# Performance work log

Measured on AMD Instinct MI355X. Metric: run time of the kernel, lower is better.

## Reference

```python
import jax, jax.numpy as jnp
import numpy as np


def setup_inputs() -> dict:
    key = jax.random.key(0)
    k1, k2, k3 = jax.random.split(key, 3)
    bs, chart_len, H = 256, 1024, 256
    num_steps, start_index = 512, 512
    chart = jax.random.normal(k1, (bs, chart_len, 2 * H), dtype=jnp.float32)
    operations = jax.random.randint(k2, (num_steps, bs, 2), 0, start_index, dtype=jnp.int64)
    U = jax.random.normal(k3, (5 * H, 2 * H), dtype=jnp.float32) * 0.05
    b = jnp.zeros((5 * H,), dtype=jnp.float32)
    return {"chart": chart, "operations": operations, "start_index": start_index, "U": U, "b": b}


def reference(chart, operations, start_index, U, b):
    H = U.shape[0] // 5
    bs = chart.shape[0]
    batch_idx = jnp.arange(bs)
    num_steps = operations.shape[0]

    def step_fn(ch, xs):
        step, ops = xs
        left = ch[batch_idx, ops[:, 0]]   # [bs, 2H]
        right = ch[batch_idx, ops[:, 1]]  # [bs, 2H]
        ccL, ccR = left[:, :H], right[:, :H]
        hh = jnp.concatenate([left[:, H:], right[:, H:]], axis=-1)  # [bs, 2H]
        preact = hh @ U.T + b  # [bs, 5H]
        i = jax.nn.sigmoid(preact[:, :H])
        fL = jax.nn.sigmoid(preact[:, H:2 * H])
        fR = jax.nn.sigmoid(preact[:, 2 * H:3 * H])
        o = jax.nn.sigmoid(preact[:, 3 * H:4 * H])
        u = jnp.tanh(preact[:, 4 * H:5 * H])
        c = fL * ccL + fR * ccR + i * u
        h = o * jnp.tanh(c)
        ch = ch.at[:, start_index + step, :].set(jnp.concatenate([c, h], axis=-1))
        return ch, None

    chart, _ = jax.lax.scan(step_fn, chart, (jnp.arange(num_steps), operations))
    return chart
```

## Files before the change

### kernel.cpp

```cpp
#include <hip/hip_runtime.h>
#include <hip/hip_bf16.h>

#define H_     256
#define TWOH_  512
#define CL_    1024
#define BS_    256
#define START_ 512

typedef float  f32x16   __attribute__((ext_vector_type(16)));
typedef short  short8_t __attribute__((ext_vector_type(8)));
typedef short  short4_t __attribute__((ext_vector_type(4)));
typedef __bf16 bf16x8   __attribute__((ext_vector_type(8)));

static __device__ __forceinline__ unsigned short f2bf(float x) {
  __hip_bfloat16 h = __float2bfloat16(x);
  return __builtin_bit_cast(unsigned short, h);
}

static __device__ __forceinline__ void gload16(const void* g, void* l) {
  __builtin_amdgcn_global_load_lds(
      (const __attribute__((address_space(1))) void*)g,
      (__attribute__((address_space(3))) void*)l, 16, 0, 0);
}

#define SCHED0() __builtin_amdgcn_sched_barrier(0)

__global__ void uconv_kernel(const float* __restrict__ U,
                             unsigned short* __restrict__ ub) {
  int tid = blockIdx.x * 256 + threadIdx.x;
  if (tid >= 1280 * 512) return;
  int n = tid >> 9, k = tid & 511;
  int g = n >> 8, j = n & 255;
  int jc = j >> 6, c = (g << 6) + (j & 63);
  ub[((jc * 320 + c) << 9) + k] = f2bf(U[tid]);
}

__global__ void hbcopy_kernel(const float4* __restrict__ chart4,
                              float4* __restrict__ out4,
                              unsigned short* __restrict__ hb) {
  const long long total = 16777216LL;
  long long tid = (long long)blockIdx.x * blockDim.x + threadIdx.x;
  for (long long e = tid; e < total; e += (long long)gridDim.x * blockDim.x) {
    long long i   = e >> 16;
    long long rem = e & 65535;
    long long off = (i << 17) + rem;
    float4 f = chart4[off];
    out4[off] = f;
    int col4 = (int)(rem & 127);
    if (col4 >= 64) {
      long long pos = rem >> 7;
      short4_t v;
      v[0] = (short)f2bf(f.x); v[1] = (short)f2bf(f.y);
      v[2] = (short)f2bf(f.z); v[3] = (short)f2bf(f.w);
      *(short4_t*)(hb + ((i * 512 + pos) * 256 + (long long)(col4 - 64) * 4)) = v;
    }
  }
}

__global__ void copy_kernel(const float4* __restrict__ src,
                            float4* __restrict__ dst) {
  long long tid = (long long)blockIdx.x * blockDim.x + threadIdx.x;
  const long long total = 16777216LL;
  for (long long e = tid; e < total; e += (long long)gridDim.x * blockDim.x) {
    long long i   = e >> 16;
    long long rem = e & 65535;
    long long off = (i << 17) + rem;
    dst[off] = src[off];
  }
}

__global__ __launch_bounds__(512, 2) void chart4_kernel(
    const float* __restrict__ chart,
    const int* __restrict__ ops,
    const unsigned short* __restrict__ ub,
    const unsigned short* __restrict__ hb,
    const float* __restrict__ bias,
    float* __restrict__ out)
{
  __shared__ unsigned short As[2][256 * 64];
  __shared__ unsigned short Bs[2][320 * 64];
  __shared__ int opsl[512];

  const int tid = threadIdx.x, lane = tid & 63, wid = tid >> 6;
  const int l31 = lane & 31, lhi = lane >> 5;
  const int wm = wid >> 1, wn = wid & 1;

  const int bx = blockIdx.x;
  const int g  = (bx & 7) * 256 + (bx >> 3);
  const int s  = g >> 2, jc = g & 3;

  opsl[tid] = ops[s * 512 + tid];
  __syncthreads();

  const int arow   = tid >> 3;
  const int slotA  = tid & 7;
  const int chunkA = slotA ^ (arow & 7);
  int opL256[4], opR256[4];
  const unsigned short* hbA[4];
  #pragma unroll
  for (int p = 0; p < 4; ++p) {
    int row = arow + p * 64;
    opL256[p] = opsl[2 * row] * 256;
    opR256[p] = opsl[2 * row + 1] * 256;
    hbA[p] = hb + ((size_t)row * 512) * 256 + chunkA * 8;
  }
  const unsigned short* ubB[5];
  #pragma unroll
  for (int p = 0; p < 5; ++p) {
    int row = arow + p * 64;
    ubB[p] = ub + (((size_t)(jc * 320 + row)) << 9) + chunkA * 8;
  }

  f32x16 acc0[5], acc1[5];
  #pragma unroll
  for (int gg = 0; gg < 5; ++gg)
    #pragma unroll
    for (int q = 0; q < 16; ++q) { acc0[gg][q] = 0.f; acc1[gg][q] = 0.f; }

#define STAGE(BUF, KT) do {                                                     \
    const int koff_ = ((KT) < 4) ? (KT) * 64 : (KT) * 64 - 256;                 \
    _Pragma("unroll")                                                           \
    for (int p = 0; p < 4; ++p) {                                               \
      const unsigned short* g_ =                                                \
          hbA[p] + (((KT) < 4) ? opL256[p] : opR256[p]) + koff_;                \
      gload16(g_, &As[BUF][(p * 512 + tid) * 8]);                               \
    }                                                                           \
    _Pragma("unroll")                                                           \
    for (int p = 0; p < 5; ++p) {                                               \
      gload16(ubB[p] + (KT) * 64, &Bs[BUF][(p * 512 + tid) * 8]);               \
    }                                                                           \
  } while (0)

  const int sw7  = l31 & 7;
  const int aro0 = (wm * 64 + l31) * 64;
  const int aro1 = aro0 + 32 * 64;
  const int bro  = (wn * 32 + l31) * 64;

#define COMPUTE(BUF) do {                                                       \
    _Pragma("unroll")                                                           \
    for (int ks = 0; ks < 4; ++ks) {                                            \
      const int ce = ((ks * 2 + lhi) ^ sw7) * 8;                                \
      bf16x8 a0 = __builtin_bit_cast(bf16x8,                                    \
          *(const short8_t*)&As[BUF][aro0 + ce]);                               \
      bf16x8 a1 = __builtin_bit_cast(bf16x8,                                    \
          *(const short8_t*)&As[BUF][aro1 + ce]);                               \
      _Pragma("unroll")                                                         \
      for (int gg = 0; gg < 5; ++gg) {                                          \
        bf16x8 b = __builtin_bit_cast(bf16x8,                                   \
            *(const short8_t*)&Bs[BUF][bro + gg * 4096 + ce]);                  \
        acc0[gg] = __builtin_amdgcn_mfma_f32_32x32x16_bf16(a0,b,acc0[gg],0,0,0);\
        acc1[gg] = __builtin_amdgcn_mfma_f32_32x32x16_bf16(a1,b,acc1[gg],0,0,0);\
      }                                                                         \
    }                                                                           \
  } while (0)

#define PHASE(BUF, KT, DOSTAGE) do {                                            \
    asm volatile("s_waitcnt vmcnt(9)" ::: "memory");                            \
    __builtin_amdgcn_s_barrier();                                               \
    SCHED0();                                                                   \
    __builtin_amdgcn_s_setprio(1);                                              \
    COMPUTE(BUF);                                                               \
    __builtin_amdgcn_s_setprio(0);                                              \
    SCHED0();                                                                   \
    __builtin_amdgcn_s_barrier();                                               \
    SCHED0();                                                                   \
    if (DOSTAGE) { STAGE(BUF, (KT) + 2); SCHED0(); }                            \
  } while (0)

  STAGE(0, 0); SCHED0();
  STAGE(1, 1); SCHED0();

  #pragma unroll
  for (int kt = 0; kt < 6; kt += 2) {
    PHASE(0, kt,     true);
    PHASE(1, kt + 1, true);
  }
  PHASE(0, 6, false);
  asm volatile("s_waitcnt vmcnt(0)" ::: "memory");
  __builtin_amdgcn_s_barrier();
  SCHED0();
  COMPUTE(1);

#undef PHASE
#undef COMPUTE
#undef STAGE

  const int jlane = jc * 64 + wn * 32 + l31;
  float bg[5];
  #pragma unroll
  for (int gg = 0; gg < 5; ++gg) bg[gg] = bias[gg * H_ + jlane];

#define EPI(ACC, MF) do {                                                       \
    _Pragma("unroll")                                                           \
    for (int q = 0; q < 16; ++q) {                                              \
      const int i_   = wm * 64 + (MF) * 32 + (q & 3) + 8 * (q >> 2) + 4 * lhi;  \
      const int opL_ = opsl[2 * i_], opR_ = opsl[2 * i_ + 1];                   \
      const float ccL_ = chart[((size_t)i_ * CL_ + opL_) * TWOH_ + jlane];      \
      const float ccR_ = chart[((size_t)i_ * CL_ + opR_) * TWOH_ + jlane];      \
      float pi_  = (ACC)[0][q] + bg[0];                                         \
      float pfL_ = (ACC)[1][q] + bg[1];                                         \
      float pfR_ = (ACC)[2][q] + bg[2];                                         \
      float po_  = (ACC)[3][q] + bg[3];                                         \
      float pu_  = (ACC)[4][q] + bg[4];                                         \
      float gi_  = 1.f / (1.f + __expf(-pi_));                                  \
      float gfL_ = 1.f / (1.f + __expf(-pfL_));                                 \
      float gfR_ = 1.f / (1.f + __expf(-pfR_));                                 \
      float go_  = 1.f / (1.f + __expf(-po_));                                  \
      float eu_  = __expf(2.f * pu_);                                           \
      float gu_  = 1.f - 2.f / (eu_ + 1.f);                                     \
      float c_   = gfL_ * ccL_ + gfR_ * ccR_ + gi_ * gu_;                       \
      float ec_  = __expf(2.f * c_);                                            \
      float th_  = 1.f - 2.f / (ec_ + 1.f);                                     \
      float h_   = go_ * th_;                                                   \
      float* orow_ = out + ((size_t)i_ * CL_ + START_ + s) * TWOH_;             \
      orow_[jlane]      = c_;                                                   \
      orow_[H_ + jlane] = h_;                                                   \
    }                                                                           \
  } while (0)

  EPI(acc0, 0);
  EPI(acc1, 1);
#undef EPI
}

__global__ __launch_bounds__(256, 2) void chart1_kernel(
    const float* __restrict__ chart,
    const int* __restrict__ ops,
    const float* __restrict__ U,
    const float* __restrict__ bias,
    float* __restrict__ out)
{
  __shared__ unsigned short As[64 * 72];
  __shared__ unsigned short Bs[320 * 72];
  __shared__ int opsl[128];

  const int tid = threadIdx.x, lane = tid & 63, wid = tid >> 6;
  const int wm = wid & 1, wn = wid >> 1;
  const int bx = blockIdx.x, jc = blockIdx.y;
  const int s = bx >> 2, ibase = (bx & 3) * 64, j0 = jc * 64;

  if (tid < 128) opsl[tid] = ops[(s * BS_ + ibase) * 2 + tid];
  __syncthreads();

  const int arow = tid >> 2, aqc = tid & 3;
  const int opL_s = opsl[2 * arow], opR_s = opsl[2 * arow + 1];
  const long long abase_i = (long long)(ibase + arow) * CL_;

  f32x16 acc[5];
  #pragma unroll
  for (int g = 0; g < 5; ++g)
    #pragma unroll
    for (int q = 0; q < 16; ++q) acc[g][q] = 0.0f;

  const int a_off  = (wm * 32 + (lane & 31)) * 72 + 8 * (lane >> 5);
  const int b_off0 = (wn * 32 + (lane & 31)) * 72 + 8 * (lane >> 5);

  for (int kt = 0; kt < 8; ++kt) {
    const int k0 = kt * 64;
    {
      const int op   = (k0 < 256) ? opL_s : opR_s;
      const int col0 = ((k0 < 256) ? 256 + k0 : k0) + aqc * 16;
      const float* src = chart + (abase_i + op) * TWOH_ + col0;
      float4 f0 = *(const float4*)(src + 0);
      float4 f1 = *(const float4*)(src + 4);
      float4 f2 = *(const float4*)(src + 8);
      float4 f3 = *(const float4*)(src + 12);
      short8_t v0, v1;
      v0[0] = (short)f2bf(f0.x); v0[1] = (short)f2bf(f0.y);
      v0[2] = (short)f2bf(f0.z); v0[3] = (short)f2bf(f0.w);
      v0[4] = (short)f2bf(f1.x); v0[5] = (short)f2bf(f1.y);
      v0[6] = (short)f2bf(f1.z); v0[7] = (short)f2bf(f1.w);
      v1[0] = (short)f2bf(f2.x); v1[1] = (short)f2bf(f2.y);
      v1[2] = (short)f2bf(f2.z); v1[3] = (short)f2bf(f2.w);
      v1[4] = (short)f2bf(f3.x); v1[5] = (short)f2bf(f3.y);
      v1[6] = (short)f2bf(f3.z); v1[7] = (short)f2bf(f3.w);
      *(short8_t*)&As[arow * 72 + aqc * 16]     = v0;
      *(short8_t*)&As[arow * 72 + aqc * 16 + 8] = v1;
    }
    #pragma unroll
    for (int cc = 0; cc < 20; ++cc) {
      int chunk = cc * 256 + tid;
      int c  = chunk >> 4;
      int ko = (chunk & 15) * 4;
      int n  = ((c >> 6) << 8) + j0 + (c & 63);
      float4 f = *(const float4*)(U + (long long)n * 512 + k0 + ko);
      short4_t v;
      v[0] = (short)f2bf(f.x); v[1] = (short)f2bf(f.y);
      v[2] = (short)f2bf(f.z); v[3] = (short)f2bf(f.w);
      *(short4_t*)&Bs[c * 72 + ko] = v;
    }
    __syncthreads();

    #pragma unroll
    for (int ks = 0; ks < 4; ++ks) {
      bf16x8 a = __builtin_bit_cast(bf16x8, *(const short8_t*)&As[a_off + ks * 16]);
      #pragma unroll
      for (int g = 0; g < 5; ++g) {
        bf16x8 b = __builtin_bit_cast(bf16x8,
            *(const short8_t*)&Bs[b_off0 + g * 64 * 72 + ks * 16]);
        acc[g] = __builtin_amdgcn_mfma_f32_32x32x16_bf16(a, b, acc[g], 0, 0, 0);
      }
    }
    __syncthreads();
  }

  const int jlane = j0 + wn * 32 + (lane & 31);
  float bg[5];
  #pragma unroll
  for (int g = 0; g < 5; ++g) bg[g] = bias[g * H_ + jlane];

  #pragma unroll
  for (int q = 0; q < 16; ++q) {
    int rl  = wm * 32 + (q & 3) + 8 * (q >> 2) + 4 * (lane >> 5);
    int i   = ibase + rl;
    int opL = opsl[2 * rl], opR = opsl[2 * rl + 1];
    float ccL = chart[((long long)i * CL_ + opL) * TWOH_ + jlane];
    float ccR = chart[((long long)i * CL_ + opR) * TWOH_ + jlane];
    float pi  = acc[0][q] + bg[0];
    float pfL = acc[1][q] + bg[1];
    float pfR = acc[2][q] + bg[2];
    float po  = acc[3][q] + bg[3];
    float pu  = acc[4][q] + bg[4];
    float gi  = 1.f / (1.f + __expf(-pi));
    float gfL = 1.f / (1.f + __expf(-pfL));
    float gfR = 1.f / (1.f + __expf(-pfR));
    float go  = 1.f / (1.f + __expf(-po));
    float eu  = __expf(2.f * pu);
    float gu  = 1.f - 2.f / (eu + 1.f);
    float c   = gfL * ccL + gfR * ccR + gi * gu;
    float ec  = __expf(2.f * c);
    float th  = 1.f - 2.f / (ec + 1.f);
    float h   = go * th;
    float* orow = out + ((long long)i * CL_ + START_ + s) * TWOH_;
    orow[jlane]      = c;
    orow[H_ + jlane] = h;
  }
}

extern "C" void kernel_launch(void* const* d_in, const int* in_sizes, int n_in,
                              void* d_out, int out_size, void* d_ws, size_t ws_size,
                              hipStream_t stream) {
  const float* chart = (const float*)d_in[0];
  const int*   ops   = (const int*)d_in[1];
  const float* U     = (const float*)d_in[3];
  const float* bias  = (const float*)d_in[4];
  float* out = (float*)d_out;

  const size_t HB_OFF   = (size_t)2 << 20;
  const size_t HB_BYTES = (size_t)256 * 512 * 256 * 2;

  if (ws_size >= HB_OFF + HB_BYTES) {
    unsigned short* ub = (unsigned short*)d_ws;
    unsigned short* hb = (unsigned short*)((char*)d_ws + HB_OFF);
    uconv_kernel<<<2560, 256, 0, stream>>>(U, ub);
    hbcopy_kernel<<<4096, 256, 0, stream>>>((const float4*)chart, (float4*)out, hb);
    chart4_kernel<<<2048, 512, 0, stream>>>(chart, ops, ub, hb, bias, out);
  } else {
    copy_kernel<<<4096, 256, 0, stream>>>((const float4*)chart, (float4*)out);
    chart1_kernel<<<dim3(2048, 4), 256, 0, stream>>>(chart, ops, U, bias, out);
  }
}
```

Before: 407.6 us.

## Loop over all four output column chunks inside one block per step

```diff
diff --git a/kernel.cpp b/kernel.cpp
--- a/kernel.cpp
+++ b/kernel.cpp
@@ -69,7 +69,7 @@
   }
 }
 
-__global__ __launch_bounds__(512, 2) void chart4_kernel(
+__global__ __launch_bounds__(512, 2) void chart5_kernel(
     const float* __restrict__ chart,
     const int* __restrict__ ops,
     const unsigned short* __restrict__ ub,
@@ -84,10 +84,7 @@
   const int tid = threadIdx.x, lane = tid & 63, wid = tid >> 6;
   const int l31 = lane & 31, lhi = lane >> 5;
   const int wm = wid >> 1, wn = wid & 1;
-
-  const int bx = blockIdx.x;
-  const int g  = (bx & 7) * 256 + (bx >> 3);
-  const int s  = g >> 2, jc = g & 3;
+  const int s = blockIdx.x;
 
   opsl[tid] = ops[s * 512 + tid];
   __syncthreads();
@@ -108,16 +105,12 @@
   #pragma unroll
   for (int p = 0; p < 5; ++p) {
     int row = arow + p * 64;
-    ubB[p] = ub + (((size_t)(jc * 320 + row)) << 9) + chunkA * 8;
+    ubB[p] = ub + ((size_t)row << 9) + chunkA * 8;
   }
 
   f32x16 acc0[5], acc1[5];
-  #pragma unroll
-  for (int gg = 0; gg < 5; ++gg)
-    #pragma unroll
-    for (int q = 0; q < 16; ++q) { acc0[gg][q] = 0.f; acc1[gg][q] = 0.f; }
-
-#define STAGE(BUF, KT) do {                                                     \
+
+#define STAGE(BUF, KT, UBO) do {                                                \
     const int koff_ = ((KT) < 4) ? (KT) * 64 : (KT) * 64 - 256;                 \
     _Pragma("unroll")                                                           \
     for (int p = 0; p < 4; ++p) {                                               \
@@ -127,7 +120,7 @@
     }                                                                           \
     _Pragma("unroll")                                                           \
     for (int p = 0; p < 5; ++p) {                                               \
-      gload16(ubB[p] + (KT) * 64, &Bs[BUF][(p * 512 + tid) * 8]);               \
+      gload16(ubB[p] + (UBO) + (KT) * 64, &Bs[BUF][(p * 512 + tid) * 8]);       \
     }                                                                           \
   } while (0)
 
@@ -154,7 +147,7 @@
     }                                                                           \
   } while (0)
 
-#define PHASE(BUF, KT, DOSTAGE) do {                                            \
+#define PHASE(BUF, KT, UBO, DOSTAGE) do {                                       \
     asm volatile("s_waitcnt vmcnt(9)" ::: "memory");                            \
     __builtin_amdgcn_s_barrier();                                               \
     SCHED0();                                                                   \
@@ -164,31 +157,47 @@
     SCHED0();                                                                   \
     __builtin_amdgcn_s_barrier();                                               \
     SCHED0();                                                                   \
-    if (DOSTAGE) { STAGE(BUF, (KT) + 2); SCHED0(); }                            \
+    if (DOSTAGE) { STAGE(BUF, (KT) + 2, UBO); SCHED0(); }                       \
   } while (0)
 
-  STAGE(0, 0); SCHED0();
-  STAGE(1, 1); SCHED0();
-
-  #pragma unroll
-  for (int kt = 0; kt < 6; kt += 2) {
-    PHASE(0, kt,     true);
-    PHASE(1, kt + 1, true);
-  }
-  PHASE(0, 6, false);
-  asm volatile("s_waitcnt vmcnt(0)" ::: "memory");
-  __builtin_amdgcn_s_barrier();
-  SCHED0();
-  COMPUTE(1);
-
-#undef PHASE
-#undef COMPUTE
-#undef STAGE
-
-  const int jlane = jc * 64 + wn * 32 + l31;
-  float bg[5];
-  #pragma unroll
-  for (int gg = 0; gg < 5; ++gg) bg[gg] = bias[gg * H_ + jlane];
+  STAGE(0, 0, 0); SCHED0();
+  STAGE(1, 1, 0); SCHED0();
+
+  for (int jc = 0; jc < 4; ++jc) {
+    const int ubo = jc * 163840;
+    const int ubn = ubo + 163840;
+
+    #pragma unroll
+    for (int gg = 0; gg < 5; ++gg)
+      #pragma unroll
+      for (int q = 0; q < 16; ++q) { acc0[gg][q] = 0.f; acc1[gg][q] = 0.f; }
+
+    PHASE(0, 0, ubo, true);
+    PHASE(1, 1, ubo, true);
+    PHASE(0, 2, ubo, true);
+    PHASE(1, 3, ubo, true);
+    PHASE(0, 4, ubo, true);
+    PHASE(1, 5, ubo, true);
+    PHASE(0, 6, ubo, false);
+    asm volatile("s_waitcnt vmcnt(0)" ::: "memory");
+    __builtin_amdgcn_s_barrier();
+    SCHED0();
+    __builtin_amdgcn_s_setprio(1);
+    COMPUTE(1);
+    __builtin_amdgcn_s_setprio(0);
+    SCHED0();
+    __builtin_amdgcn_s_barrier();
+    SCHED0();
+
+    if (jc < 3) {
+      STAGE(0, 0, ubn); SCHED0();
+      STAGE(1, 1, ubn); SCHED0();
+    }
+
+    const int jlane = jc * 64 + wn * 32 + l31;
+    float bg[5];
+    #pragma unroll
+    for (int gg = 0; gg < 5; ++gg) bg[gg] = bias[gg * H_ + jlane];
 
 #define EPI(ACC, MF) do {                                                       \
     _Pragma("unroll")                                                           \
@@ -218,9 +227,13 @@
     }                                                                           \
   } while (0)
 
-  EPI(acc0, 0);
-  EPI(acc1, 1);
+    EPI(acc0, 0);
+    EPI(acc1, 1);
 #undef EPI
+  }
+#undef PHASE
+#undef COMPUTE
+#undef STAGE
 }
 
 __global__ __launch_bounds__(256, 2) void chart1_kernel(
@@ -354,7 +367,7 @@
     unsigned short* hb = (unsigned short*)((char*)d_ws + HB_OFF);
     uconv_kernel<<<2560, 256, 0, stream>>>(U, ub);
     hbcopy_kernel<<<4096, 256, 0, stream>>>((const float4*)chart, (float4*)out, hb);
-    chart4_kernel<<<2048, 512, 0, stream>>>(chart, ops, ub, hb, bias, out);
+    chart5_kernel<<<512, 512, 0, stream>>>(chart, ops, ub, hb, bias, out);
   } else {
     copy_kernel<<<4096, 256, 0, stream>>>((const float4*)chart, (float4*)out);
     chart1_kernel<<<dim3(2048, 4), 256, 0, stream>>>(chart, ops, U, bias, out);
```

Result: slower. 704.7 us (+72.9%).

## Shrink GEMM tiles and load U fragments directly from global in MFMA order

Applied to the files above, without the earlier changes.

```diff
diff --git a/kernel.cpp b/kernel.cpp
--- a/kernel.cpp
+++ b/kernel.cpp
@@ -25,14 +25,30 @@
 
 #define SCHED0() __builtin_amdgcn_sched_barrier(0)
 
-__global__ void uconv_kernel(const float* __restrict__ U,
-                             unsigned short* __restrict__ ub) {
-  int tid = blockIdx.x * 256 + threadIdx.x;
-  if (tid >= 1280 * 512) return;
-  int n = tid >> 9, k = tid & 511;
-  int g = n >> 8, j = n & 255;
-  int jc = j >> 6, c = (g << 6) + (j & 63);
-  ub[((jc * 320 + c) << 9) + k] = f2bf(U[tid]);
+__global__ void uconv2_kernel(const float* __restrict__ U,
+                              unsigned short* __restrict__ ubF) {
+  int c = blockIdx.x * 256 + threadIdx.x;
+  if (c >= 81920) return;
+  int lane = c & 63;
+  int t1 = c >> 6;
+  int ks = t1 & 3;
+  int t2 = t1 >> 2;
+  int kt = t2 & 7;
+  int t3 = t2 >> 3;
+  int g  = t3 % 5;
+  int jw = t3 / 5;
+  int jc = jw >> 1, wn = jw & 1;
+  int n  = g * 256 + jc * 64 + wn * 32 + (lane & 31);
+  int k  = kt * 64 + (ks * 2 + (lane >> 5)) * 8;
+  const float* src = U + (size_t)n * 512 + k;
+  float4 f0 = *(const float4*)(src);
+  float4 f1 = *(const float4*)(src + 4);
+  short8_t v;
+  v[0] = (short)f2bf(f0.x); v[1] = (short)f2bf(f0.y);
+  v[2] = (short)f2bf(f0.z); v[3] = (short)f2bf(f0.w);
+  v[4] = (short)f2bf(f1.x); v[5] = (short)f2bf(f1.y);
+  v[6] = (short)f2bf(f1.z); v[7] = (short)f2bf(f1.w);
+  *(short8_t*)(ubF + (size_t)c * 8) = v;
 }
 
 __global__ void hbcopy_kernel(const float4* __restrict__ chart4,
@@ -69,46 +85,42 @@
   }
 }
 
-__global__ __launch_bounds__(512, 2) void chart4_kernel(
+__global__ __launch_bounds__(128) void chart6_kernel(
     const float* __restrict__ chart,
     const int* __restrict__ ops,
-    const unsigned short* __restrict__ ub,
+    const unsigned short* __restrict__ ubF,
     const unsigned short* __restrict__ hb,
     const float* __restrict__ bias,
     float* __restrict__ out)
 {
-  __shared__ unsigned short As[2][256 * 64];
-  __shared__ unsigned short Bs[2][320 * 64];
-  __shared__ int opsl[512];
-
-  const int tid = threadIdx.x, lane = tid & 63, wid = tid >> 6;
+  __shared__ unsigned short As[2][64 * 64];
+  __shared__ int opsl[128];
+
+  const int tid = threadIdx.x, lane = tid & 63, wn = tid >> 6;
   const int l31 = lane & 31, lhi = lane >> 5;
-  const int wm = wid >> 1, wn = wid & 1;
 
   const int bx = blockIdx.x;
-  const int g  = (bx & 7) * 256 + (bx >> 3);
-  const int s  = g >> 2, jc = g & 3;
-
-  opsl[tid] = ops[s * 512 + tid];
+  const int g  = (bx & 7) * 1024 + (bx >> 3);
+  const int s  = g >> 4, mg = (g >> 2) & 3, jc = g & 3;
+
+  opsl[tid] = ops[((size_t)s * BS_ + mg * 64) * 2 + tid];
   __syncthreads();
 
-  const int arow   = tid >> 3;
-  const int slotA  = tid & 7;
-  const int chunkA = slotA ^ (arow & 7);
+  const int chunkA = (tid & 7) ^ ((tid >> 3) & 7);
   int opL256[4], opR256[4];
   const unsigned short* hbA[4];
   #pragma unroll
   for (int p = 0; p < 4; ++p) {
-    int row = arow + p * 64;
-    opL256[p] = opsl[2 * row] * 256;
-    opR256[p] = opsl[2 * row + 1] * 256;
-    hbA[p] = hb + ((size_t)row * 512) * 256 + chunkA * 8;
-  }
-  const unsigned short* ubB[5];
+    int rl = p * 16 + (tid >> 3);
+    opL256[p] = opsl[2 * rl] * 256;
+    opR256[p] = opsl[2 * rl + 1] * 256;
+    hbA[p] = hb + ((size_t)(mg * 64 + rl) * 512) * 256 + chunkA * 8;
+  }
+
+  const unsigned short* bpB[5];
   #pragma unroll
   for (int p = 0; p < 5; ++p) {
-    int row = arow + p * 64;
-    ubB[p] = ub + (((size_t)(jc * 320 + row)) << 9) + chunkA * 8;
+    bpB[p] = ubF + ((size_t)(((jc * 2 + wn) * 5 + p) * 2048 + lane)) * 8;
   }
 
   f32x16 acc0[5], acc1[5];
@@ -123,20 +135,15 @@
     for (int p = 0; p < 4; ++p) {                                               \
       const unsigned short* g_ =                                                \
           hbA[p] + (((KT) < 4) ? opL256[p] : opR256[p]) + koff_;                \
-      gload16(g_, &As[BUF][(p * 512 + tid) * 8]);                               \
-    }                                                                           \
-    _Pragma("unroll")                                                           \
-    for (int p = 0; p < 5; ++p) {                                               \
-      gload16(ubB[p] + (KT) * 64, &Bs[BUF][(p * 512 + tid) * 8]);               \
+      gload16(g_, &As[BUF][(p * 128 + tid) * 8]);                               \
     }                                                                           \
   } while (0)
 
+  const int aro0 = l31 * 64;
+  const int aro1 = (32 + l31) * 64;
   const int sw7  = l31 & 7;
-  const int aro0 = (wm * 64 + l31) * 64;
-  const int aro1 = aro0 + 32 * 64;
-  const int bro  = (wn * 32 + l31) * 64;
-
-#define COMPUTE(BUF) do {                                                       \
+
+#define COMPUTE(BUF, KT) do {                                                   \
     _Pragma("unroll")                                                           \
     for (int ks = 0; ks < 4; ++ks) {                                            \
       const int ce = ((ks * 2 + lhi) ^ sw7) * 8;                                \
@@ -147,7 +154,7 @@
       _Pragma("unroll")                                                         \
       for (int gg = 0; gg < 5; ++gg) {                                          \
         bf16x8 b = __builtin_bit_cast(bf16x8,                                   \
-            *(const short8_t*)&Bs[BUF][bro + gg * 4096 + ce]);                  \
+            *(const short8_t*)(bpB[gg] + ((KT) * 4 + ks) * 512));               \
         acc0[gg] = __builtin_amdgcn_mfma_f32_32x32x16_bf16(a0,b,acc0[gg],0,0,0);\
         acc1[gg] = __builtin_amdgcn_mfma_f32_32x32x16_bf16(a1,b,acc1[gg],0,0,0);\
       }                                                                         \
@@ -155,12 +162,10 @@
   } while (0)
 
 #define PHASE(BUF, KT, DOSTAGE) do {                                            \
-    asm volatile("s_waitcnt vmcnt(9)" ::: "memory");                            \
+    asm volatile("s_waitcnt vmcnt(4)" ::: "memory");                            \
     __builtin_amdgcn_s_barrier();                                               \
     SCHED0();                                                                   \
-    __builtin_amdgcn_s_setprio(1);                                              \
-    COMPUTE(BUF);                                                               \
-    __builtin_amdgcn_s_setprio(0);                                              \
+    COMPUTE(BUF, KT);                                                           \
     SCHED0();                                                                   \
     __builtin_amdgcn_s_barrier();                                               \
     SCHED0();                                                                   \
@@ -170,16 +175,17 @@
   STAGE(0, 0); SCHED0();
   STAGE(1, 1); SCHED0();
 
-  #pragma unroll
-  for (int kt = 0; kt < 6; kt += 2) {
-    PHASE(0, kt,     true);
-    PHASE(1, kt + 1, true);
-  }
+  PHASE(0, 0, true);
+  PHASE(1, 1, true);
+  PHASE(0, 2, true);
+  PHASE(1, 3, true);
+  PHASE(0, 4, true);
+  PHASE(1, 5, true);
   PHASE(0, 6, false);
   asm volatile("s_waitcnt vmcnt(0)" ::: "memory");
   __builtin_amdgcn_s_barrier();
   SCHED0();
-  COMPUTE(1);
+  COMPUTE(1, 7);
 
 #undef PHASE
 #undef COMPUTE
@@ -193,8 +199,9 @@
 #define EPI(ACC, MF) do {                                                       \
     _Pragma("unroll")                                                           \
     for (int q = 0; q < 16; ++q) {                                              \
-      const int i_   = wm * 64 + (MF) * 32 + (q & 3) + 8 * (q >> 2) + 4 * lhi;  \
-      const int opL_ = opsl[2 * i_], opR_ = opsl[2 * i_ + 1];                   \
+      const int rl_  = (MF) * 32 + (q & 3) + 8 * (q >> 2) + 4 * lhi;            \
+      const int i_   = mg * 64 + rl_;                                           \
+      const int opL_ = opsl[2 * rl_], opR_ = opsl[2 * rl_ + 1];                 \
       const float ccL_ = chart[((size_t)i_ * CL_ + opL_) * TWOH_ + jlane];      \
       const float ccR_ = chart[((size_t)i_ * CL_ + opR_) * TWOH_ + jlane];      \
       float pi_  = (ACC)[0][q] + bg[0];                                         \
@@ -350,11 +357,11 @@
   const size_t HB_BYTES = (size_t)256 * 512 * 256 * 2;
 
   if (ws_size >= HB_OFF + HB_BYTES) {
-    unsigned short* ub = (unsigned short*)d_ws;
-    unsigned short* hb = (unsigned short*)((char*)d_ws + HB_OFF);
-    uconv_kernel<<<2560, 256, 0, stream>>>(U, ub);
+    unsigned short* ubF = (unsigned short*)d_ws;
+    unsigned short* hb  = (unsigned short*)((char*)d_ws + HB_OFF);
+    uconv2_kernel<<<320, 256, 0, stream>>>(U, ubF);
     hbcopy_kernel<<<4096, 256, 0, stream>>>((const float4*)chart, (float4*)out, hb);
-    chart4_kernel<<<2048, 512, 0, stream>>>(chart, ops, ub, hb, bias, out);
+    chart6_kernel<<<8192, 128, 0, stream>>>(chart, ops, ubF, hb, bias, out);
   } else {
     copy_kernel<<<4096, 256, 0, stream>>>((const float4*)chart, (float4*)out);
     chart1_kernel<<<dim3(2048, 4), 256, 0, stream>>>(chart, ops, U, bias, out);
```

Result: slower. 472.4 us (+15.9%).
